# Performance work log

Measured on AMD Instinct MI355X. Metric: run time of the kernel, lower is better.

Reference implementation:

```python
import jax, jax.numpy as jnp
import numpy as np

S, B, H = 2048, 32, 1024

def setup_inputs() -> dict:
    key = jax.random.key(0)
    ks = jax.random.split(key, 5)
    hidden = jax.random.normal(ks[0], (B, H), dtype=jnp.float32)
    encoder_outputs = jax.random.normal(ks[1], (S, B, H), dtype=jnp.float32)
    source_lengths = jax.random.randint(ks[2], (B,), 1, S + 1, dtype=jnp.int32)
    attn_w = jax.random.normal(ks[3], (H, 2 * H), dtype=jnp.float32) / np.sqrt(2 * H)
    attn_b = jnp.zeros((H,), dtype=jnp.float32)
    v = jax.random.uniform(ks[4], (H,), dtype=jnp.float32)
    return {"hidden": hidden, "encoder_outputs": encoder_outputs,
            "source_lengths": source_lengths, "attn_w": attn_w,
            "attn_b": attn_b, "v": v}

def reference(hidden, encoder_outputs, source_lengths, attn_w, attn_b, v):
    s, b, h = encoder_outputs.shape
    # Broadcast decoder hidden over source positions: (S,B,H)
    hid = jnp.broadcast_to(hidden[None, :, :], (s, b, h))
    cat = jnp.concatenate([hid, encoder_outputs], axis=2)          # (S,B,2H)
    energy = jnp.tanh(jnp.einsum('sbk,hk->sbh', cat, attn_w) + attn_b)  # (S,B,H)
    scores = jnp.einsum('sbh,h->bs', energy, v)                     # (B,S)
    mask = jnp.arange(s)[None, :] < source_lengths[:, None]         # (B,S)
    scores = jnp.where(mask, scores, jnp.float32(-1e10))
    attention_weights = jax.nn.softmax(scores, axis=1)              # (B,S)
    context = jnp.einsum('bs,sbh->bh', attention_weights, encoder_outputs)
    return context, attention_weights
```

## Files before the change

kernel.cpp:

```cpp
#include <hip/hip_runtime.h>

#define S_DIM 2048
#define B_DIM 32
#define H_DIM 1024
#define ROWS  (S_DIM * B_DIM)

typedef __attribute__((ext_vector_type(4))) float    f32x4;
typedef __attribute__((ext_vector_type(8))) _Float16 f16x8;
typedef __attribute__((ext_vector_type(2))) __fp16   h16x2;

__device__ __forceinline__ unsigned short f16_bits(float f) {
  union { _Float16 h; unsigned short u; } cv;
  cv.h = (_Float16)f;
  return cv.u;
}

__device__ __forceinline__ float fast_tanh(float x) {
  x = fminf(15.0f, fmaxf(-15.0f, x));
  float z = __expf(-2.0f * x);
  return (1.0f - z) * __builtin_amdgcn_rcpf(1.0f + z);
}

__device__ __forceinline__ void load_lds16(const void* g, void* l) {
  __builtin_amdgcn_global_load_lds(
      (const __attribute__((address_space(1))) unsigned int*)g,
      (__attribute__((address_space(3))) unsigned int*)l, 16, 0, 0);
}

__device__ __forceinline__ f32x4 gload16(const float* p) {
  f32x4 r;
  asm volatile("global_load_dwordx4 %0, %1, off" : "=v"(r) : "v"(p) : "memory");
  return r;
}

#define PRIO1 __builtin_amdgcn_s_setprio(1)
#define PRIO0 __builtin_amdgcn_s_setprio(0)
#define SBAR  __builtin_amdgcn_sched_barrier(0)
#define BAR   __builtin_amdgcn_s_barrier
#define VMC8() do { asm volatile("s_waitcnt vmcnt(8)" ::: "memory"); \
                    __builtin_amdgcn_sched_barrier(0); } while (0)
#define VMC0() do { asm volatile("s_waitcnt vmcnt(0)" ::: "memory"); \
                    __builtin_amdgcn_sched_barrier(0); } while (0)
#define LGKM0() do { asm volatile("s_waitcnt lgkmcnt(0)" ::: "memory"); \
                     __builtin_amdgcn_sched_barrier(0); } while (0)

__global__ void prep_kernel(const float* __restrict__ hidden,
                            const float* __restrict__ attn_w,
                            const float* __restrict__ attn_b,
                            float* __restrict__ hp,
                            unsigned short* __restrict__ Bp,
                            float* __restrict__ scores,
                            float* __restrict__ ctx) {
  int bid = blockIdx.x, tid = threadIdx.x;
  if (bid < 64) {
    int hl = tid >> 4;
    int kp = tid & 15;
    int h  = bid * 16 + hl;
    const f32x4* wrow = (const f32x4*)(attn_w + (size_t)h * (2 * H_DIM)) + kp * 16;
    f32x4 w[16];
#pragma unroll
    for (int j = 0; j < 16; ++j) w[j] = wrow[j];
    float bias = attn_b[h];
    for (int b = 0; b < B_DIM; ++b) {
      const f32x4* xrow = (const f32x4*)(hidden + (size_t)b * H_DIM) + kp * 16;
      float s = 0.f;
#pragma unroll
      for (int j = 0; j < 16; ++j) {
        f32x4 x = xrow[j];
        s = fmaf(w[j].x, x.x, s); s = fmaf(w[j].y, x.y, s);
        s = fmaf(w[j].z, x.z, s); s = fmaf(w[j].w, x.w, s);
      }
      s += __shfl_xor(s, 1); s += __shfl_xor(s, 2);
      s += __shfl_xor(s, 4); s += __shfl_xor(s, 8);
      if (kp == 0) hp[(size_t)b * H_DIM + h] = s + bias;
    }
  } else if (bid < 576) {
    int id   = (bid - 64) * 256 + tid;
    int p    = id & 7;
    int r    = (id >> 3) & 127;
    int half = (id >> 10) & 1;
    int kt   = (id >> 11) & 15;
    int g    = id >> 15;
    int sub  = p ^ (r & 7);
    int n    = g * 256 + half * 128 + r;
    const float* src = attn_w + (size_t)n * (2 * H_DIM) + H_DIM + kt * 64 + sub * 8;
    f32x4 a = *(const f32x4*)src;
    f32x4 b = *(const f32x4*)(src + 4);
    ushort4 lo, hi;
    lo.x = f16_bits(a.x); lo.y = f16_bits(a.y); lo.z = f16_bits(a.z); lo.w = f16_bits(a.w);
    hi.x = f16_bits(b.x); hi.y = f16_bits(b.y); hi.z = f16_bits(b.z); hi.w = f16_bits(b.w);
    *(ushort4*)(Bp + (size_t)id * 8)     = lo;
    *(ushort4*)(Bp + (size_t)id * 8 + 4) = hi;
  } else if (bid < 640) {
    int idx = (bid - 576) * 256 + tid;
    *(f32x4*)(scores + (size_t)idx * 4) = (f32x4){0.f, 0.f, 0.f, 0.f};
  } else {
    int idx = (bid - 640) * 256 + tid;
    *(f32x4*)(ctx + (size_t)idx * 4) = (f32x4){0.f, 0.f, 0.f, 0.f};
  }
}

__global__ __launch_bounds__(512, 2)
void gemm_scores_kernel(const float* __restrict__ enc,
                        const unsigned short* __restrict__ Bp,
                        const float* __restrict__ hp,
                        const float* __restrict__ v,
                        float* __restrict__ scores) {
  __shared__ __align__(16) unsigned short Asl[2][16384];
  __shared__ __align__(16) unsigned short Bsl[2][16384];

  const int tid  = threadIdx.x;
  const int lane = tid & 63;
  const int wid  = tid >> 6;
  const int wm   = wid >> 2;
  const int wn   = wid & 3;
  const int m16  = lane & 15;
  const int quad = lane >> 4;
  const int swz  = m16 & 7;

  const int bid  = blockIdx.x;
  const int xcd  = bid & 7;
  const int slot = bid >> 3;
  const int t    = xcd * 32 + (slot >> 2);
  const int g    = slot & 3;

  const int c0  = ((0 * 4 + quad) ^ swz) * 8;
  const int c1  = ((1 * 4 + quad) ^ swz) * 8;
  const int rdA = wm * 8192 + m16 * 64;
  const int rdB = (wn >> 1) * 8192 + ((wn & 1) * 64 + m16) * 64;

  const int r0 = tid >> 3;
  const int s0 = (tid & 7) ^ (r0 & 7);
  const int r1 = (512 + tid) >> 3;
  const int s1 = ((512 + tid) & 7) ^ (r1 & 7);
  const int aoff0 = r0 * H_DIM + s0 * 8;
  const int aoff1 = r1 * H_DIM + s1 * 8;
  const float* encT = enc + (size_t)t * 256 * H_DIM;
  const unsigned short* BpG = Bp + (size_t)g * 262144;

  f32x4 acc[8][4];
#pragma unroll
  for (int i = 0; i < 8; ++i)
#pragma unroll
    for (int j = 0; j < 4; ++j) acc[i][j] = (f32x4){0.f, 0.f, 0.f, 0.f};

  f16x8 af[4][2];
  f16x8 bf[2][2];
  f32x4 rh0[4], rh1[4];

#define ISSUE_A(HH, KT, R)                                                     \
  {                                                                            \
    const float* s_ = encT + (size_t)(HH)*131072 + (KT)*64;                    \
    R[0] = gload16(s_ + aoff0);                                                \
    R[1] = gload16(s_ + aoff0 + 4);                                            \
    R[2] = gload16(s_ + aoff1);                                                \
    R[3] = gload16(s_ + aoff1 + 4);                                            \
  }

#define CVT_WRITE(HH, R, DST)                                                  \
  {                                                                            \
    union { f16x8 v8; h16x2 h2[4]; } pk;                                       \
    pk.h2[0] = __builtin_amdgcn_cvt_pkrtz(R[0].x, R[0].y);                     \
    pk.h2[1] = __builtin_amdgcn_cvt_pkrtz(R[0].z, R[0].w);                     \
    pk.h2[2] = __builtin_amdgcn_cvt_pkrtz(R[1].x, R[1].y);                     \
    pk.h2[3] = __builtin_amdgcn_cvt_pkrtz(R[1].z, R[1].w);                     \
    *(f16x8*)((DST) + (HH)*8192 + tid * 8) = pk.v8;                            \
    pk.h2[0] = __builtin_amdgcn_cvt_pkrtz(R[2].x, R[2].y);                     \
    pk.h2[1] = __builtin_amdgcn_cvt_pkrtz(R[2].z, R[2].w);                     \
    pk.h2[2] = __builtin_amdgcn_cvt_pkrtz(R[3].x, R[3].y);                     \
    pk.h2[3] = __builtin_amdgcn_cvt_pkrtz(R[3].z, R[3].w);                     \
    *(f16x8*)((DST) + (HH)*8192 + 4096 + tid * 8) = pk.v8;                     \
  }

#define STAGE_B(HH, KT, DST)                                                   \
  {                                                                            \
    const unsigned short* s_ = BpG + (KT)*16384 + (HH)*8192 + tid * 8;         \
    load_lds16(s_, (DST) + (HH)*8192 + tid * 8);                               \
    load_lds16(s_ + 4096, (DST) + (HH)*8192 + 4096 + tid * 8);                 \
  }

#define A_READ(MH, SRC)                                                        \
  _Pragma("unroll")                                                            \
  for (int f = 0; f < 4; ++f) {                                                \
    af[f][0] = *(const f16x8*)((SRC) + rdA + ((MH)*64 + f * 16) * 64 + c0);    \
    af[f][1] = *(const f16x8*)((SRC) + rdA + ((MH)*64 + f * 16) * 64 + c1);    \
  }

#define B_READ(NH, SRC)                                                        \
  _Pragma("unroll")                                                            \
  for (int f = 0; f < 2; ++f) {                                                \
    bf[f][0] = *(const f16x8*)((SRC) + rdB + ((NH)*32 + f * 16) * 64 + c0);    \
    bf[f][1] = *(const f16x8*)((SRC) + rdB + ((NH)*32 + f * 16) * 64 + c1);    \
  }

#define MFMA_Q(MH, NH)                                                         \
  _Pragma("unroll")                                                            \
  for (int mf = 0; mf < 4; ++mf) {                                             \
    _Pragma("unroll")                                                          \
    for (int nf = 0; nf < 2; ++nf) {                                           \
      acc[(MH)*4 + mf][(NH)*2 + nf] = __builtin_amdgcn_mfma_f32_16x16x32_f16(  \
          af[mf][0], bf[nf][0], acc[(MH)*4 + mf][(NH)*2 + nf], 0, 0, 0);       \
      acc[(MH)*4 + mf][(NH)*2 + nf] = __builtin_amdgcn_mfma_f32_16x16x32_f16(  \
          af[mf][1], bf[nf][1], acc[(MH)*4 + mf][(NH)*2 + nf], 0, 0, 0);       \
    }                                                                          \
  }

  ISSUE_A(0, 0, rh0);
  ISSUE_A(1, 0, rh1);
  STAGE_B(0, 0, &Bsl[0][0]);
  STAGE_B(1, 0, &Bsl[0][0]);
  VMC8();
  CVT_WRITE(0, rh0, &Asl[0][0]);
  ISSUE_A(0, 1, rh0);
  VMC8();
  CVT_WRITE(1, rh1, &Asl[0][0]);
  ISSUE_A(1, 1, rh1);
  VMC8();
  LGKM0();
  BAR(); SBAR;

#define TILE(CUR, T)                                                           \
  {                                                                            \
    unsigned short* Ac = &Asl[CUR][0];                                         \
    unsigned short* Bc = &Bsl[CUR][0];                                         \
    unsigned short* An = &Asl[(CUR) ^ 1][0];                                   \
    unsigned short* Bn = &Bsl[(CUR) ^ 1][0];                                   \
    const int ktB = ((T) + 1 < 16) ? (T) + 1 : 15;                             \
    const int ktA = ((T) + 2 < 16) ? (T) + 2 : 15;                             \
                                                           \
    A_READ(0, Ac); B_READ(0, Bc);                                              \
    STAGE_B(0, ktB, Bn);                                                       \
    BAR(); LGKM0();                                                            \
    PRIO1; MFMA_Q(0, 0); PRIO0;                                                \
    BAR(); SBAR;                                                               \
                                               \
    B_READ(1, Bc);                                                             \
    STAGE_B(1, ktB, Bn);                                                       \
    BAR(); LGKM0();                                                            \
    PRIO1; MFMA_Q(0, 1); PRIO0;                                                \
    BAR(); SBAR;                                                               \
             \
    A_READ(1, Ac);                                                             \
    VMC8();                                                                    \
    CVT_WRITE(0, rh0, An);                                                     \
    ISSUE_A(0, ktA, rh0);                                                      \
    BAR(); LGKM0();                                                            \
    PRIO1; MFMA_Q(1, 1); PRIO0;                                                \
    BAR(); SBAR;                                                               \
           \
    B_READ(0, Bc);                                                             \
    VMC8();                                                                    \
    CVT_WRITE(1, rh1, An);                                                     \
    ISSUE_A(1, ktA, rh1);                                                      \
    BAR(); LGKM0();                                                            \
    PRIO1; MFMA_Q(1, 0); PRIO0;                                                \
    VMC8();                                                                    \
    BAR(); SBAR;                                                               \
  }

#pragma unroll 1
  for (int tt = 0; tt < 16; tt += 2) {
    TILE(0, tt);
    TILE(1, tt + 1);
  }

  VMC0();

  const int row0 = t * 256 + wm * 128;
  const int col0 = g * 256 + wn * 64;
#pragma unroll
  for (int a = 0; a < 8; ++a) {
    const int rbase = row0 + (a >> 2) * 64 + (a & 3) * 16 + quad * 4;
#pragma unroll
    for (int reg = 0; reg < 4; ++reg) {
      int row_g = rbase + reg;
      int bb    = row_g & 31;
      int ss    = row_g >> 5;
      float psum = 0.f;
#pragma unroll
      for (int b2 = 0; b2 < 4; ++b2) {
        int col = col0 + (b2 >> 1) * 32 + (b2 & 1) * 16 + m16;
        float e = acc[a][b2][reg] + hp[bb * H_DIM + col];
        e = fast_tanh(e);
        psum = fmaf(e, v[col], psum);
      }
      psum += __shfl_xor(psum, 1);
      psum += __shfl_xor(psum, 2);
      psum += __shfl_xor(psum, 4);
      psum += __shfl_xor(psum, 8);
      if (m16 == 0) atomicAdd(&scores[bb * S_DIM + ss], psum);
    }
  }
#undef TILE
#undef MFMA_Q
#undef B_READ
#undef A_READ
#undef STAGE_B
#undef CVT_WRITE
#undef ISSUE_A
}

__global__ void softmax_kernel(const float* __restrict__ scores,
                               const int* __restrict__ lens,
                               float* __restrict__ wout) {
  int b = blockIdx.x, tid = threadIdx.x;
  int len = lens[b];
  float vals[8];
  float m = -3.0e38f;
#pragma unroll
  for (int i = 0; i < 8; ++i) {
    int s = i * 256 + tid;
    float x = scores[b * S_DIM + s];
    vals[i] = (s < len) ? x : -3.0e38f;
    m = fmaxf(m, vals[i]);
  }
#pragma unroll
  for (int off = 32; off > 0; off >>= 1) m = fmaxf(m, __shfl_xor(m, off));
  __shared__ float redm[4], reds[4];
  int wid = tid >> 6, lane = tid & 63;
  if (lane == 0) redm[wid] = m;
  __syncthreads();
  m = fmaxf(fmaxf(redm[0], redm[1]), fmaxf(redm[2], redm[3]));

  float e[8];
  float sum = 0.f;
#pragma unroll
  for (int i = 0; i < 8; ++i) {
    int s = i * 256 + tid;
    e[i] = (s < len) ? __expf(vals[i] - m) : 0.f;
    sum += e[i];
  }
#pragma unroll
  for (int off = 32; off > 0; off >>= 1) sum += __shfl_xor(sum, off);
  if (lane == 0) reds[wid] = sum;
  __syncthreads();
  sum = reds[0] + reds[1] + reds[2] + reds[3];
  float inv = 1.0f / sum;
#pragma unroll
  for (int i = 0; i < 8; ++i)
    wout[b * S_DIM + i * 256 + tid] = e[i] * inv;
}

__global__ void context_kernel(const float* __restrict__ enc,
                               const float* __restrict__ wts,
                               const int* __restrict__ lens,
                               float* __restrict__ ctx) {
  int sc = blockIdx.x;
  int b  = blockIdx.y;
  int len = lens[b];
  int s0 = sc * 128;
  if (s0 >= len) return;
  int cnt = min(128, len - s0);
  int tid = threadIdx.x;
  f32x4 acc = (f32x4){0.f, 0.f, 0.f, 0.f};
  const float* wrow = wts + (size_t)b * S_DIM + s0;
#pragma unroll 4
  for (int i = 0; i < cnt; ++i) {
    float w = wrow[i];
    f32x4 e = *(const f32x4*)(enc + ((size_t)(s0 + i) * B_DIM + b) * H_DIM + tid * 4);
    acc.x = fmaf(w, e.x, acc.x);
    acc.y = fmaf(w, e.y, acc.y);
    acc.z = fmaf(w, e.z, acc.z);
    acc.w = fmaf(w, e.w, acc.w);
  }
  float* dst = ctx + (size_t)b * H_DIM + tid * 4;
  atomicAdd(dst + 0, acc.x);
  atomicAdd(dst + 1, acc.y);
  atomicAdd(dst + 2, acc.z);
  atomicAdd(dst + 3, acc.w);
}

extern "C" void kernel_launch(void* const* d_in, const int* in_sizes, int n_in,
                              void* d_out, int out_size, void* d_ws, size_t ws_size,
                              hipStream_t stream) {
  const float* hidden = (const float*)d_in[0];
  const float* enc    = (const float*)d_in[1];
  const int*   lens   = (const int*)d_in[2];
  const float* attn_w = (const float*)d_in[3];
  const float* attn_b = (const float*)d_in[4];
  const float* v      = (const float*)d_in[5];

  float* out_ctx = (float*)d_out;
  float* out_w   = (float*)d_out + B_DIM * H_DIM;

  char* p = (char*)d_ws;
  float* scores = (float*)p;               p += (size_t)B_DIM * S_DIM * 4;
  float* hp     = (float*)p;               p += (size_t)B_DIM * H_DIM * 4;
  unsigned short* Bp = (unsigned short*)p;

  hipLaunchKernelGGL(prep_kernel, dim3(672), dim3(256), 0, stream,
                     hidden, attn_w, attn_b, hp, Bp, scores, out_ctx);
  hipLaunchKernelGGL(gemm_scores_kernel, dim3(1024), dim3(512), 0, stream,
                     enc, Bp, hp, v, scores);
  hipLaunchKernelGGL(softmax_kernel, dim3(B_DIM), dim3(256), 0, stream,
                     scores, lens, out_w);
  hipLaunchKernelGGL(context_kernel, dim3(16, B_DIM), dim3(256), 0, stream,
                     enc, out_w, lens, out_ctx);
}
```

Before: 628.3 us.

## Pre-convert encoder outputs to swizzled fp16 and stage A via direct LDS loads

Measured after the change: 641.7 us. +2.1%, slower.

```diff
diff --git a/kernel.cpp b/kernel.cpp
--- a/kernel.cpp
+++ b/kernel.cpp
@@ -37,9 +37,7 @@
 #define PRIO0 __builtin_amdgcn_s_setprio(0)
 #define SBAR  __builtin_amdgcn_sched_barrier(0)
 #define BAR   __builtin_amdgcn_s_barrier
-#define VMC8() do { asm volatile("s_waitcnt vmcnt(8)" ::: "memory"); \
-                    __builtin_amdgcn_sched_barrier(0); } while (0)
-#define VMC0() do { asm volatile("s_waitcnt vmcnt(0)" ::: "memory"); \
+#define VMC(N) do { asm volatile("s_waitcnt vmcnt(" #N ")" ::: "memory"); \
                     __builtin_amdgcn_sched_barrier(0); } while (0)
 #define LGKM0() do { asm volatile("s_waitcnt lgkmcnt(0)" ::: "memory"); \
                      __builtin_amdgcn_sched_barrier(0); } while (0)
@@ -47,8 +45,10 @@
 __global__ void prep_kernel(const float* __restrict__ hidden,
                             const float* __restrict__ attn_w,
                             const float* __restrict__ attn_b,
+                            const float* __restrict__ enc,
                             float* __restrict__ hp,
                             unsigned short* __restrict__ Bp,
+                            unsigned short* __restrict__ encT16,
                             float* __restrict__ scores,
                             float* __restrict__ ctx) {
   int bid = blockIdx.x, tid = threadIdx.x;
@@ -94,14 +94,30 @@
   } else if (bid < 640) {
     int idx = (bid - 576) * 256 + tid;
     *(f32x4*)(scores + (size_t)idx * 4) = (f32x4){0.f, 0.f, 0.f, 0.f};
-  } else {
+  } else if (bid < 672) {
     int idx = (bid - 640) * 256 + tid;
     *(f32x4*)(ctx + (size_t)idx * 4) = (f32x4){0.f, 0.f, 0.f, 0.f};
+  } else {
+    int cg  = (bid - 672) * 256 + tid;
+    int q   = cg & 2047;
+    int ktt = (cg >> 11) & 15;
+    int tt  = cg >> 15;
+    int r   = q >> 3;
+    int p   = q & 7;
+    int sub = p ^ (r & 7);
+    const float* src = enc + ((size_t)tt * 256 + r) * H_DIM + ktt * 64 + sub * 8;
+    f32x4 a = *(const f32x4*)src;
+    f32x4 b = *(const f32x4*)(src + 4);
+    ushort4 lo, hi;
+    lo.x = f16_bits(a.x); lo.y = f16_bits(a.y); lo.z = f16_bits(a.z); lo.w = f16_bits(a.w);
+    hi.x = f16_bits(b.x); hi.y = f16_bits(b.y); hi.z = f16_bits(b.z); hi.w = f16_bits(b.w);
+    *(ushort4*)(encT16 + (size_t)cg * 8)     = lo;
+    *(ushort4*)(encT16 + (size_t)cg * 8 + 4) = hi;
   }
 }
 
 __global__ __launch_bounds__(512, 2)
-void gemm_scores_kernel(const float* __restrict__ enc,
+void gemm_scores_kernel(const unsigned short* __restrict__ encT16,
                         const unsigned short* __restrict__ Bp,
                         const float* __restrict__ hp,
                         const float* __restrict__ v,
@@ -124,19 +140,11 @@
   const int t    = xcd * 32 + (slot >> 2);
   const int g    = slot & 3;
 
-  const int c0  = ((0 * 4 + quad) ^ swz) * 8;
-  const int c1  = ((1 * 4 + quad) ^ swz) * 8;
-  const int rdA = wm * 8192 + m16 * 64;
-  const int rdB = (wn >> 1) * 8192 + ((wn & 1) * 64 + m16) * 64;
-
-  const int r0 = tid >> 3;
-  const int s0 = (tid & 7) ^ (r0 & 7);
-  const int r1 = (512 + tid) >> 3;
-  const int s1 = ((512 + tid) & 7) ^ (r1 & 7);
-  const int aoff0 = r0 * H_DIM + s0 * 8;
-  const int aoff1 = r1 * H_DIM + s1 * 8;
-  const float* encT = enc + (size_t)t * 256 * H_DIM;
-  const unsigned short* BpG = Bp + (size_t)g * 262144;
+  const int c0 = ((0 * 4 + quad) ^ swz) * 8;
+  const int c1 = ((1 * 4 + quad) ^ swz) * 8;
+
+  const unsigned short* Abase = encT16 + (size_t)t * 262144;
+  const unsigned short* Bbase = Bp     + (size_t)g * 262144;
 
   f32x4 acc[8][4];
 #pragma unroll
@@ -146,53 +154,41 @@
 
   f16x8 af[4][2];
   f16x8 bf[2][2];
-  f32x4 rh0[4], rh1[4];
-
-#define ISSUE_A(HH, KT, R)                                                     \
-  {                                                                            \
-    const float* s_ = encT + (size_t)(HH)*131072 + (KT)*64;                    \
-    R[0] = gload16(s_ + aoff0);                                                \
-    R[1] = gload16(s_ + aoff0 + 4);                                            \
-    R[2] = gload16(s_ + aoff1);                                                \
-    R[3] = gload16(s_ + aoff1 + 4);                                            \
-  }
-
-#define CVT_WRITE(HH, R, DST)                                                  \
-  {                                                                            \
-    union { f16x8 v8; h16x2 h2[4]; } pk;                                       \
-    pk.h2[0] = __builtin_amdgcn_cvt_pkrtz(R[0].x, R[0].y);                     \
-    pk.h2[1] = __builtin_amdgcn_cvt_pkrtz(R[0].z, R[0].w);                     \
-    pk.h2[2] = __builtin_amdgcn_cvt_pkrtz(R[1].x, R[1].y);                     \
-    pk.h2[3] = __builtin_amdgcn_cvt_pkrtz(R[1].z, R[1].w);                     \
-    *(f16x8*)((DST) + (HH)*8192 + tid * 8) = pk.v8;                            \
-    pk.h2[0] = __builtin_amdgcn_cvt_pkrtz(R[2].x, R[2].y);                     \
-    pk.h2[1] = __builtin_amdgcn_cvt_pkrtz(R[2].z, R[2].w);                     \
-    pk.h2[2] = __builtin_amdgcn_cvt_pkrtz(R[3].x, R[3].y);                     \
-    pk.h2[3] = __builtin_amdgcn_cvt_pkrtz(R[3].z, R[3].w);                     \
-    *(f16x8*)((DST) + (HH)*8192 + 4096 + tid * 8) = pk.v8;                     \
-  }
-
-#define STAGE_B(HH, KT, DST)                                                   \
-  {                                                                            \
-    const unsigned short* s_ = BpG + (KT)*16384 + (HH)*8192 + tid * 8;         \
-    load_lds16(s_, (DST) + (HH)*8192 + tid * 8);                               \
-    load_lds16(s_ + 4096, (DST) + (HH)*8192 + 4096 + tid * 8);                 \
-  }
-
+
+#define STAGE_A_L0(KT, DST)                                                    \
+  {                                                                            \
+    const unsigned short* s_ = Abase + (size_t)(KT)*16384;                     \
+    load_lds16(s_ + (size_t)tid * 8,          (DST) + tid * 8);                \
+    load_lds16(s_ + (size_t)(1024 + tid) * 8, (DST) + (1024 + tid) * 8);       \
+  }
+#define STAGE_A_L1(KT, DST)                                                    \
+  {                                                                            \
+    const unsigned short* s_ = Abase + (size_t)(KT)*16384;                     \
+    load_lds16(s_ + (size_t)(512 + tid) * 8,  (DST) + (512 + tid) * 8);        \
+    load_lds16(s_ + (size_t)(1536 + tid) * 8, (DST) + (1536 + tid) * 8);       \
+  }
+#define STAGE_B4(KT, DST)                                                      \
+  {                                                                            \
+    const unsigned short* s_ = Bbase + (size_t)(KT)*16384;                     \
+    load_lds16(s_ + (size_t)tid * 8,          (DST) + tid * 8);                \
+    load_lds16(s_ + (size_t)(512 + tid) * 8,  (DST) + (512 + tid) * 8);        \
+    load_lds16(s_ + (size_t)(1024 + tid) * 8, (DST) + (1024 + tid) * 8);       \
+    load_lds16(s_ + (size_t)(1536 + tid) * 8, (DST) + (1536 + tid) * 8);       \
+  }
 #define A_READ(MH, SRC)                                                        \
   _Pragma("unroll")                                                            \
   for (int f = 0; f < 4; ++f) {                                                \
-    af[f][0] = *(const f16x8*)((SRC) + rdA + ((MH)*64 + f * 16) * 64 + c0);    \
-    af[f][1] = *(const f16x8*)((SRC) + rdA + ((MH)*64 + f * 16) * 64 + c1);    \
-  }
-
+    int r_ = wm * 128 + (MH)*64 + f * 16 + m16;                                \
+    af[f][0] = *(const f16x8*)((SRC) + r_ * 64 + c0);                          \
+    af[f][1] = *(const f16x8*)((SRC) + r_ * 64 + c1);                          \
+  }
 #define B_READ(NH, SRC)                                                        \
   _Pragma("unroll")                                                            \
   for (int f = 0; f < 2; ++f) {                                                \
-    bf[f][0] = *(const f16x8*)((SRC) + rdB + ((NH)*32 + f * 16) * 64 + c0);    \
-    bf[f][1] = *(const f16x8*)((SRC) + rdB + ((NH)*32 + f * 16) * 64 + c1);    \
-  }
-
+    int n_ = wn * 64 + (NH)*32 + f * 16 + m16;                                 \
+    bf[f][0] = *(const f16x8*)((SRC) + n_ * 64 + c0);                          \
+    bf[f][1] = *(const f16x8*)((SRC) + n_ * 64 + c1);                          \
+  }
 #define MFMA_Q(MH, NH)                                                         \
   _Pragma("unroll")                                                            \
   for (int mf = 0; mf < 4; ++mf) {                                             \
@@ -205,18 +201,10 @@
     }                                                                          \
   }
 
-  ISSUE_A(0, 0, rh0);
-  ISSUE_A(1, 0, rh1);
-  STAGE_B(0, 0, &Bsl[0][0]);
-  STAGE_B(1, 0, &Bsl[0][0]);
-  VMC8();
-  CVT_WRITE(0, rh0, &Asl[0][0]);
-  ISSUE_A(0, 1, rh0);
-  VMC8();
-  CVT_WRITE(1, rh1, &Asl[0][0]);
-  ISSUE_A(1, 1, rh1);
-  VMC8();
-  LGKM0();
+  STAGE_A_L0(0, &Asl[0][0]);
+  STAGE_B4(0, &Bsl[0][0]);
+  STAGE_A_L1(0, &Asl[0][0]);
+  VMC(2);
   BAR(); SBAR;
 
 #define TILE(CUR, T)                                                           \
@@ -225,36 +213,31 @@
     unsigned short* Bc = &Bsl[CUR][0];                                         \
     unsigned short* An = &Asl[(CUR) ^ 1][0];                                   \
     unsigned short* Bn = &Bsl[(CUR) ^ 1][0];                                   \
-    const int ktB = ((T) + 1 < 16) ? (T) + 1 : 15;                             \
-    const int ktA = ((T) + 2 < 16) ? (T) + 2 : 15;                             \
+    const int ktn = ((T) + 1 < 16) ? (T) + 1 : 15;    \
                                                            \
     A_READ(0, Ac); B_READ(0, Bc);                                              \
-    STAGE_B(0, ktB, Bn);                                                       \
+    STAGE_A_L0(ktn, An);                                                       \
     BAR(); LGKM0();                                                            \
     PRIO1; MFMA_Q(0, 0); PRIO0;                                                \
     BAR(); SBAR;                                                               \
                                                \
     B_READ(1, Bc);                                                             \
-    STAGE_B(1, ktB, Bn);                                                       \
+    STAGE_B4(ktn, Bn);                                                         \
+    VMC(6);                    \
     BAR(); LGKM0();                                                            \
     PRIO1; MFMA_Q(0, 1); PRIO0;                                                \
     BAR(); SBAR;                                                               \
-             \
+                                               \
     A_READ(1, Ac);                                                             \
-    VMC8();                                                                    \
-    CVT_WRITE(0, rh0, An);                                                     \
-    ISSUE_A(0, ktA, rh0);                                                      \
+    STAGE_A_L1(ktn, An);                                                       \
     BAR(); LGKM0();                                                            \
     PRIO1; MFMA_Q(1, 1); PRIO0;                                                \
     BAR(); SBAR;                                                               \
-           \
+                                                           \
     B_READ(0, Bc);                                                             \
-    VMC8();                                                                    \
-    CVT_WRITE(1, rh1, An);                                                     \
-    ISSUE_A(1, ktA, rh1);                                                      \
+    VMC(2);           \
     BAR(); LGKM0();                                                            \
     PRIO1; MFMA_Q(1, 0); PRIO0;                                                \
-    VMC8();                                                                    \
     BAR(); SBAR;                                                               \
   }
 
@@ -264,7 +247,8 @@
     TILE(1, tt + 1);
   }
 
-  VMC0();
+  asm volatile("s_waitcnt vmcnt(0)" ::: "memory");
+  SBAR;
 
   const int row0 = t * 256 + wm * 128;
   const int col0 = g * 256 + wn * 64;
@@ -295,6 +279,192 @@
 #undef MFMA_Q
 #undef B_READ
 #undef A_READ
+#undef STAGE_B4
+#undef STAGE_A_L1
+#undef STAGE_A_L0
+}
+
+__global__ __launch_bounds__(512, 2)
+void gemm_scores_fallback(const float* __restrict__ enc,
+                          const unsigned short* __restrict__ Bp,
+                          const float* __restrict__ hp,
+                          const float* __restrict__ v,
+                          float* __restrict__ scores) {
+  __shared__ __align__(16) unsigned short Asl[2][16384];
+  __shared__ __align__(16) unsigned short Bsl[2][16384];
+  const int tid  = threadIdx.x;
+  const int lane = tid & 63;
+  const int wid  = tid >> 6;
+  const int wm   = wid >> 2;
+  const int wn   = wid & 3;
+  const int m16  = lane & 15;
+  const int quad = lane >> 4;
+  const int swz  = m16 & 7;
+  const int bid  = blockIdx.x;
+  const int xcd  = bid & 7;
+  const int slot = bid >> 3;
+  const int t    = xcd * 32 + (slot >> 2);
+  const int g    = slot & 3;
+  const int c0  = ((0 * 4 + quad) ^ swz) * 8;
+  const int c1  = ((1 * 4 + quad) ^ swz) * 8;
+  const int rdA = wm * 8192 + m16 * 64;
+  const int rdB = (wn >> 1) * 8192 + ((wn & 1) * 64 + m16) * 64;
+  const int r0 = tid >> 3;
+  const int s0 = (tid & 7) ^ (r0 & 7);
+  const int r1 = (512 + tid) >> 3;
+  const int s1 = ((512 + tid) & 7) ^ (r1 & 7);
+  const int aoff0 = r0 * H_DIM + s0 * 8;
+  const int aoff1 = r1 * H_DIM + s1 * 8;
+  const float* encT = enc + (size_t)t * 256 * H_DIM;
+  const unsigned short* BpG = Bp + (size_t)g * 262144;
+
+  f32x4 acc[8][4];
+#pragma unroll
+  for (int i = 0; i < 8; ++i)
+#pragma unroll
+    for (int j = 0; j < 4; ++j) acc[i][j] = (f32x4){0.f, 0.f, 0.f, 0.f};
+  f16x8 af[4][2];
+  f16x8 bf[2][2];
+  f32x4 rh0[4], rh1[4];
+
+#define ISSUE_A(HH, KT, R)                                                     \
+  {                                                                            \
+    const float* s_ = encT + (size_t)(HH)*131072 + (KT)*64;                    \
+    R[0] = gload16(s_ + aoff0);                                                \
+    R[1] = gload16(s_ + aoff0 + 4);                                            \
+    R[2] = gload16(s_ + aoff1);                                                \
+    R[3] = gload16(s_ + aoff1 + 4);                                            \
+  }
+#define CVT_WRITE(HH, R, DST)                                                  \
+  {                                                                            \
+    union { f16x8 v8; h16x2 h2[4]; } pk;                                       \
+    pk.h2[0] = __builtin_amdgcn_cvt_pkrtz(R[0].x, R[0].y);                     \
+    pk.h2[1] = __builtin_amdgcn_cvt_pkrtz(R[0].z, R[0].w);                     \
+    pk.h2[2] = __builtin_amdgcn_cvt_pkrtz(R[1].x, R[1].y);                     \
+    pk.h2[3] = __builtin_amdgcn_cvt_pkrtz(R[1].z, R[1].w);                     \
+    *(f16x8*)((DST) + (HH)*8192 + tid * 8) = pk.v8;                            \
+    pk.h2[0] = __builtin_amdgcn_cvt_pkrtz(R[2].x, R[2].y);                     \
+    pk.h2[1] = __builtin_amdgcn_cvt_pkrtz(R[2].z, R[2].w);                     \
+    pk.h2[2] = __builtin_amdgcn_cvt_pkrtz(R[3].x, R[3].y);                     \
+    pk.h2[3] = __builtin_amdgcn_cvt_pkrtz(R[3].z, R[3].w);                     \
+    *(f16x8*)((DST) + (HH)*8192 + 4096 + tid * 8) = pk.v8;                     \
+  }
+#define STAGE_B(HH, KT, DST)                                                   \
+  {                                                                            \
+    const unsigned short* s_ = BpG + (KT)*16384 + (HH)*8192 + tid * 8;         \
+    load_lds16(s_, (DST) + (HH)*8192 + tid * 8);                               \
+    load_lds16(s_ + 4096, (DST) + (HH)*8192 + 4096 + tid * 8);                 \
+  }
+#define A_READF(MH, SRC)                                                       \
+  _Pragma("unroll")                                                            \
+  for (int f = 0; f < 4; ++f) {                                                \
+    af[f][0] = *(const f16x8*)((SRC) + rdA + ((MH)*64 + f * 16) * 64 + c0);    \
+    af[f][1] = *(const f16x8*)((SRC) + rdA + ((MH)*64 + f * 16) * 64 + c1);    \
+  }
+#define B_READF(NH, SRC)                                                       \
+  _Pragma("unroll")                                                            \
+  for (int f = 0; f < 2; ++f) {                                                \
+    bf[f][0] = *(const f16x8*)((SRC) + rdB + ((NH)*32 + f * 16) * 64 + c0);    \
+    bf[f][1] = *(const f16x8*)((SRC) + rdB + ((NH)*32 + f * 16) * 64 + c1);    \
+  }
+#define MFMA_QF(MH, NH)                                                        \
+  _Pragma("unroll")                                                            \
+  for (int mf = 0; mf < 4; ++mf) {                                             \
+    _Pragma("unroll")                                                          \
+    for (int nf = 0; nf < 2; ++nf) {                                           \
+      acc[(MH)*4 + mf][(NH)*2 + nf] = __builtin_amdgcn_mfma_f32_16x16x32_f16(  \
+          af[mf][0], bf[nf][0], acc[(MH)*4 + mf][(NH)*2 + nf], 0, 0, 0);       \
+      acc[(MH)*4 + mf][(NH)*2 + nf] = __builtin_amdgcn_mfma_f32_16x16x32_f16(  \
+          af[mf][1], bf[nf][1], acc[(MH)*4 + mf][(NH)*2 + nf], 0, 0, 0);       \
+    }                                                                          \
+  }
+
+  ISSUE_A(0, 0, rh0);
+  ISSUE_A(1, 0, rh1);
+  STAGE_B(0, 0, &Bsl[0][0]);
+  STAGE_B(1, 0, &Bsl[0][0]);
+  VMC(8);
+  CVT_WRITE(0, rh0, &Asl[0][0]);
+  ISSUE_A(0, 1, rh0);
+  VMC(8);
+  CVT_WRITE(1, rh1, &Asl[0][0]);
+  ISSUE_A(1, 1, rh1);
+  VMC(8);
+  LGKM0();
+  BAR(); SBAR;
+
+#define TILEF(CUR, T)                                                          \
+  {                                                                            \
+    unsigned short* Ac = &Asl[CUR][0];                                         \
+    unsigned short* Bc = &Bsl[CUR][0];                                         \
+    unsigned short* An = &Asl[(CUR) ^ 1][0];                                   \
+    unsigned short* Bn = &Bsl[(CUR) ^ 1][0];                                   \
+    const int ktB = ((T) + 1 < 16) ? (T) + 1 : 15;                             \
+    const int ktA = ((T) + 2 < 16) ? (T) + 2 : 15;                             \
+    A_READF(0, Ac); B_READF(0, Bc);                                            \
+    STAGE_B(0, ktB, Bn);                                                       \
+    BAR(); LGKM0();                                                            \
+    PRIO1; MFMA_QF(0, 0); PRIO0;                                               \
+    BAR(); SBAR;                                                               \
+    B_READF(1, Bc);                                                            \
+    STAGE_B(1, ktB, Bn);                                                       \
+    BAR(); LGKM0();                                                            \
+    PRIO1; MFMA_QF(0, 1); PRIO0;                                               \
+    BAR(); SBAR;                                                               \
+    A_READF(1, Ac);                                                            \
+    VMC(8);                                                                    \
+    CVT_WRITE(0, rh0, An);                                                     \
+    ISSUE_A(0, ktA, rh0);                                                      \
+    BAR(); LGKM0();                                                            \
+    PRIO1; MFMA_QF(1, 1); PRIO0;                                               \
+    BAR(); SBAR;                                                               \
+    B_READF(0, Bc);                                                            \
+    VMC(8);                                                                    \
+    CVT_WRITE(1, rh1, An);                                                     \
+    ISSUE_A(1, ktA, rh1);                                                      \
+    BAR(); LGKM0();                                                            \
+    PRIO1; MFMA_QF(1, 0); PRIO0;                                               \
+    VMC(8);                                                                    \
+    BAR(); SBAR;                                                               \
+  }
+
+#pragma unroll 1
+  for (int tt = 0; tt < 16; tt += 2) {
+    TILEF(0, tt);
+    TILEF(1, tt + 1);
+  }
+  asm volatile("s_waitcnt vmcnt(0)" ::: "memory");
+  SBAR;
+
+  const int row0 = t * 256 + wm * 128;
+  const int col0 = g * 256 + wn * 64;
+#pragma unroll
+  for (int a = 0; a < 8; ++a) {
+    const int rbase = row0 + (a >> 2) * 64 + (a & 3) * 16 + quad * 4;
+#pragma unroll
+    for (int reg = 0; reg < 4; ++reg) {
+      int row_g = rbase + reg;
+      int bb    = row_g & 31;
+      int ss    = row_g >> 5;
+      float psum = 0.f;
+#pragma unroll
+      for (int b2 = 0; b2 < 4; ++b2) {
+        int col = col0 + (b2 >> 1) * 32 + (b2 & 1) * 16 + m16;
+        float e = acc[a][b2][reg] + hp[bb * H_DIM + col];
+        e = fast_tanh(e);
+        psum = fmaf(e, v[col], psum);
+      }
+      psum += __shfl_xor(psum, 1);
+      psum += __shfl_xor(psum, 2);
+      psum += __shfl_xor(psum, 4);
+      psum += __shfl_xor(psum, 8);
+      if (m16 == 0) atomicAdd(&scores[bb * S_DIM + ss], psum);
+    }
+  }
+#undef TILEF
+#undef MFMA_QF
+#undef B_READF
+#undef A_READF
 #undef STAGE_B
 #undef CVT_WRITE
 #undef ISSUE_A
@@ -386,12 +556,23 @@
   char* p = (char*)d_ws;
   float* scores = (float*)p;               p += (size_t)B_DIM * S_DIM * 4;
   float* hp     = (float*)p;               p += (size_t)B_DIM * H_DIM * 4;
-  unsigned short* Bp = (unsigned short*)p;
-
-  hipLaunchKernelGGL(prep_kernel, dim3(672), dim3(256), 0, stream,
-                     hidden, attn_w, attn_b, hp, Bp, scores, out_ctx);
-  hipLaunchKernelGGL(gemm_scores_kernel, dim3(1024), dim3(512), 0, stream,
-                     enc, Bp, hp, v, scores);
+  unsigned short* Bp = (unsigned short*)p; p += (size_t)2 * 1024 * 1024;
+  unsigned short* enc16 = (unsigned short*)p;
+
+  const size_t need = (size_t)B_DIM * S_DIM * 4 + (size_t)B_DIM * H_DIM * 4 +
+                      (size_t)2 * 1024 * 1024 + (size_t)ROWS * H_DIM * 2;
+
+  if (ws_size >= need) {
+    hipLaunchKernelGGL(prep_kernel, dim3(672 + 32768), dim3(256), 0, stream,
+                       hidden, attn_w, attn_b, enc, hp, Bp, enc16, scores, out_ctx);
+    hipLaunchKernelGGL(gemm_scores_kernel, dim3(1024), dim3(512), 0, stream,
+                       enc16, Bp, hp, v, scores);
+  } else {
+    hipLaunchKernelGGL(prep_kernel, dim3(672), dim3(256), 0, stream,
+                       hidden, attn_w, attn_b, enc, hp, Bp, enc16, scores, out_ctx);
+    hipLaunchKernelGGL(gemm_scores_fallback, dim3(1024), dim3(512), 0, stream,
+                       enc, Bp, hp, v, scores);
+  }
   hipLaunchKernelGGL(softmax_kernel, dim3(B_DIM), dim3(256), 0, stream,
                      scores, lens, out_w);
   hipLaunchKernelGGL(context_kernel, dim3(16, B_DIM), dim3(256), 0, stream,
```
